# Kernel tuning notes

Hardware: AMD Instinct MI355X
Metric: run time of the kernel (lower is better)

Reference implementation:

```python
import jax, jax.numpy as jnp
import numpy as np

N = 100000          # nodes
E = 1600000         # edges per adjacency (avg degree 16)
DIMS = [256, 128, 64]
ALPHA = 0.8
WD = 1e-4


def setup_inputs() -> dict:
    key = jax.random.key(0)
    ks = jax.random.split(key, 11)
    X = jax.random.normal(ks[0], (N, DIMS[0]), jnp.float32)
    rows = jax.random.randint(ks[1], (E,), 0, N, jnp.int32)
    cols = jax.random.randint(ks[2], (E,), 0, N, jnp.int32)
    prune_rows = jax.random.randint(ks[3], (E,), 0, N, jnp.int32)
    prune_cols = jax.random.randint(ks[4], (E,), 0, N, jnp.int32)
    # learned params (torch.randn init, scaled 0.1 for fp32 numeric headroom)
    W0 = jax.random.normal(ks[5], (DIMS[0], DIMS[1]), jnp.float32) * 0.1
    W1 = jax.random.normal(ks[6], (DIMS[1], DIMS[2]), jnp.float32) * 0.1
    v00 = jax.random.normal(ks[7], (DIMS[1], 1), jnp.float32) * 0.1
    v01 = jax.random.normal(ks[8], (DIMS[1], 1), jnp.float32) * 0.1
    pv00 = jax.random.normal(ks[9], (DIMS[1], 1), jnp.float32) * 0.1
    pv01 = jax.random.normal(ks[10], (DIMS[1], 1), jnp.float32) * 0.1
    return {"X": X, "W0": W0, "W1": W1, "v00": v00, "v01": v01,
            "pv00": pv00, "pv01": pv01, "rows": rows, "cols": cols,
            "prune_rows": prune_rows, "prune_cols": prune_cols}


def _edge_softmax(rows, logits, n):
    # row-wise softmax over sparse edge logits
    m = jax.ops.segment_max(logits, rows, num_segments=n)
    e = jnp.exp(logits - m[rows])
    s = jax.ops.segment_sum(e, rows, num_segments=n)
    return e / s[rows]


def _attention(rows, cols, H, va, vb, n):
    # logit_e = (H @ va)[src_e] + (H @ vb)[dst_e]  (binary adjacency values)
    f1 = (H @ va)[:, 0]
    f2 = (H @ vb)[:, 0]
    return _edge_softmax(rows, f1[rows] + f2[cols], n)


def _spmm(rows, cols, vals, H, n):
    # out[i] = sum_{e: rows[e]==i} vals[e] * H[cols[e]]
    return jax.ops.segment_sum(vals[:, None] * H[cols], rows, num_segments=n)


def reference(X, W0, W1, v00, v01, pv00, pv01, rows, cols, prune_rows, prune_cols):
    n = X.shape[0]
    # ---- encoder ----
    H1 = X @ W0                                   # layer 0 projection
    c = _attention(rows, cols, H1, v00, v01, n)   # C[0]
    pc = _attention(prune_rows, prune_cols, H1, pv00, pv01, n)  # prune_C[0]
    H1a = (1.0 - ALPHA) * _spmm(rows, cols, c, H1, n) \
        + ALPHA * _spmm(prune_rows, prune_cols, pc, H1, n)
    H1a = jax.nn.elu(H1a)                         # nonlinear, layer 0 != last
    H_enc = H1a @ W1                              # layer 1 == last: no attention
    # ---- decoder ----
    D = H_enc @ W1.T                              # layer 1
    D = (1.0 - ALPHA) * _spmm(rows, cols, c, D, n) \
        + ALPHA * _spmm(prune_rows, prune_cols, pc, D, n)
    D = jax.nn.elu(D)                             # nonlinear, layer 1 != 0
    X_ = D @ W0.T                                 # layer 0: plain matmul
    # ---- loss ----
    loss = jnp.sqrt(jnp.sum((X - X_) ** 2)) \
         + WD * (jnp.sum(W0 ** 2) + jnp.sum(W1 ** 2))
    return (loss, H_enc, X_)
```

## Files before the change

### kernel.cpp

```cpp
#include <hip/hip_runtime.h>
#include <math.h>

#define N_NODES 100000
#define N_EDGES 1600000
#define TOT (2 * N_NODES)
#define SCAN_NB 256
#define SCAN_CH 4
#define RPB 25000

static inline int cdiv(long a, long b) { return (int)((a + b - 1) / b); }

typedef unsigned int uint;
typedef unsigned short ushort;
typedef __attribute__((ext_vector_type(8))) short short8v;
typedef __attribute__((ext_vector_type(4))) float f32x4;

__device__ inline float bf2f(uint u) { return __uint_as_float(u << 16); }
__device__ inline ushort f2bf(float f) {
    uint u = __float_as_uint(f);
    uint r = ((u >> 16) & 1u) + 0x7fffu;
    return (ushort)((u + r) >> 16);
}

template <int K, int M, bool AF32, int OUT, bool ELU, bool LOSS>
__global__ __launch_bounds__(256) void gemm_mfma(const void* __restrict__ Av,
                                                 const ushort* __restrict__ Bcm,
                                                 void* __restrict__ Cv,
                                                 void* __restrict__ Cv2,
                                                 const float* __restrict__ Xref,
                                                 float* __restrict__ partial,
                                                 int nrows) {
    constexpr int BM = 128;
    constexpr int KP = K + 8;
    constexpr int NCT = M / 16;
    __shared__ ushort Blds[M * KP];
    __shared__ ushort Alds[BM * 32];
    const int w = threadIdx.x >> 6;
    const int l = threadIdx.x & 63;
    const int rowg = l & 15;
    const int kg = l >> 4;
    const int rbase = blockIdx.x * BM;
    {
        const uint4* src = reinterpret_cast<const uint4*>(Bcm);
        uint4* dst = reinterpret_cast<uint4*>(Blds);
        const int total = M * KP / 8;
        for (int i = threadIdx.x; i < total; i += 256) dst[i] = src[i];
    }
    f32x4 acc[2][NCT] = {};
    for (int k0 = 0; k0 < K; k0 += 32) {
        __syncthreads();
        int r = threadIdx.x >> 1;
        int kk = (threadIdx.x & 1) * 16;
        int rg = min(rbase + r, nrows - 1);
        if (AF32) {
            const float* A = (const float*)Av;
            const float4* src = reinterpret_cast<const float4*>(A + (size_t)rg * K + k0 + kk);
            ushort* dst = &Alds[r * 32 + kk];
#pragma unroll
            for (int q = 0; q < 4; ++q) {
                float4 v = src[q];
                dst[4 * q + 0] = f2bf(v.x); dst[4 * q + 1] = f2bf(v.y);
                dst[4 * q + 2] = f2bf(v.z); dst[4 * q + 3] = f2bf(v.w);
            }
        } else {
            const ushort* A = (const ushort*)Av;
            const uint4* src = reinterpret_cast<const uint4*>(A + (size_t)rg * K + k0 + kk);
            uint4* dst = reinterpret_cast<uint4*>(&Alds[r * 32 + kk]);
            dst[0] = src[0];
            dst[1] = src[1];
        }
        __syncthreads();
#pragma unroll
        for (int rt = 0; rt < 2; ++rt) {
            short8v af = *reinterpret_cast<const short8v*>(
                &Alds[(w * 32 + rt * 16 + rowg) * 32 + kg * 8]);
#pragma unroll
            for (int ct = 0; ct < NCT; ++ct) {
                short8v bf = *reinterpret_cast<const short8v*>(
                    &Blds[(ct * 16 + rowg) * KP + k0 + kg * 8]);
                acc[rt][ct] = __builtin_amdgcn_mfma_f32_16x16x32_bf16(
                    af, bf, acc[rt][ct], 0, 0, 0);
            }
        }
    }
    float lsum = 0.f;
#pragma unroll
    for (int rt = 0; rt < 2; ++rt) {
#pragma unroll
        for (int q = 0; q < 4; ++q) {
            int r = rbase + w * 32 + rt * 16 + kg * 4 + q;
            if (r >= nrows) continue;
#pragma unroll
            for (int ct = 0; ct < NCT; ++ct) {
                float o = acc[rt][ct][q];
                if (ELU) o = o > 0.f ? o : expm1f(o);
                int col = ct * 16 + rowg;
                if (OUT == 0 || OUT == 3) ((float*)Cv)[(size_t)r * M + col] = o;
                if (OUT == 2) ((ushort*)Cv)[(size_t)r * M + col] = f2bf(o);
                if (OUT == 3) ((ushort*)Cv2)[(size_t)r * M + col] = f2bf(o);
                if (LOSS) {
                    float d = o - Xref[(size_t)r * 256 + col];
                    lsum += d * d;
                }
            }
        }
    }
    if (LOSS) {
        __shared__ float smRed[4];
#pragma unroll
        for (int off = 32; off > 0; off >>= 1) lsum += __shfl_down(lsum, off);
        __syncthreads();
        if (l == 0) smRed[w] = lsum;
        __syncthreads();
        if (threadIdx.x == 0)
            partial[blockIdx.x] = smRed[0] + smRed[1] + smRed[2] + smRed[3];
    }
}

__global__ __launch_bounds__(256) void prepB1_kernel(const float* __restrict__ W0,
                                                     ushort* __restrict__ B) {
    int i = blockIdx.x * 256 + threadIdx.x;
    if (i >= 256 * 128) return;
    int k = i / 128, m = i - k * 128;
    B[m * 264 + k] = f2bf(W0[i]);
}
__global__ __launch_bounds__(256) void prepB5_kernel(const float* __restrict__ W1,
                                                     ushort* __restrict__ B) {
    int i = blockIdx.x * 256 + threadIdx.x;
    if (i >= 128 * 64) return;
    int k = i / 64, m = i - k * 64;
    B[m * 136 + k] = f2bf(W1[i]);
}
__global__ __launch_bounds__(256) void prepB7_kernel(const float* __restrict__ W1,
                                                     ushort* __restrict__ B) {
    int i = blockIdx.x * 256 + threadIdx.x;
    if (i >= 128 * 64) return;
    int m = i / 64, k = i - m * 64;
    B[m * 72 + k] = f2bf(W1[i]);
}
__global__ __launch_bounds__(256) void prepB8_kernel(const float* __restrict__ W0,
                                                     ushort* __restrict__ B) {
    int i = blockIdx.x * 256 + threadIdx.x;
    if (i >= 256 * 128) return;
    int m = i / 128, k = i - m * 128;
    B[m * 136 + k] = f2bf(W0[i]);
}

__global__ __launch_bounds__(256) void attn_f4_kernel(const ushort* __restrict__ Hb,
                                                      const float* __restrict__ va,
                                                      const float* __restrict__ vb,
                                                      const float* __restrict__ pva,
                                                      const float* __restrict__ pvb,
                                                      float* __restrict__ f1,
                                                      float* __restrict__ f2,
                                                      float* __restrict__ pf1,
                                                      float* __restrict__ pf2) {
    int wid = (blockIdx.x * 256 + threadIdx.x) >> 6;
    int lane = threadIdx.x & 63;
    if (wid >= N_NODES) return;
    uint hv = reinterpret_cast<const uint*>(Hb + (size_t)wid * 128)[lane];
    float x0 = bf2f(hv & 0xffffu);
    float x1 = bf2f(hv >> 16);
    int k = 2 * lane;
    float a = x0 * va[k] + x1 * va[k + 1];
    float b = x0 * vb[k] + x1 * vb[k + 1];
    float pa = x0 * pva[k] + x1 * pva[k + 1];
    float pb = x0 * pvb[k] + x1 * pvb[k + 1];
#pragma unroll
    for (int off = 32; off > 0; off >>= 1) {
        a += __shfl_down(a, off);
        b += __shfl_down(b, off);
        pa += __shfl_down(pa, off);
        pb += __shfl_down(pb, off);
    }
    if (lane == 0) { f1[wid] = a; f2[wid] = b; pf1[wid] = pa; pf2[wid] = pb; }
}

__global__ __launch_bounds__(256) void hist2_kernel(const int* __restrict__ rows,
                                                    const int* __restrict__ prows,
                                                    int* __restrict__ deg) {
    int e = blockIdx.x * 256 + threadIdx.x;
    if (e >= 2 * N_EDGES) return;
    int b = e < N_EDGES ? rows[e] * 2 : prows[e - N_EDGES] * 2 + 1;
    atomicAdd(&deg[b], 1);
}

__device__ inline int pad8(int d) { return (d + 7) & ~7; }

__global__ __launch_bounds__(256) void scan1_kernel(const int* __restrict__ deg,
                                                    int* __restrict__ bsum) {
    __shared__ int sm[256];
    int base = (blockIdx.x * 256 + threadIdx.x) * SCAN_CH;
    int s = 0;
#pragma unroll
    for (int i = 0; i < SCAN_CH; ++i) {
        int idx = base + i;
        if (idx < TOT) s += pad8(deg[idx]);
    }
    sm[threadIdx.x] = s;
    __syncthreads();
    for (int off = 128; off > 0; off >>= 1) {
        if (threadIdx.x < off) sm[threadIdx.x] += sm[threadIdx.x + off];
        __syncthreads();
    }
    if (threadIdx.x == 0) bsum[blockIdx.x] = sm[0];
}

__global__ void scan2_kernel(int* __restrict__ bsum) {
    if (threadIdx.x != 0) return;
    int run = 0;
    for (int i = 0; i < SCAN_NB; ++i) {
        int t = bsum[i];
        bsum[i] = run;
        run += t;
    }
}

__global__ __launch_bounds__(256) void scan3_kernel(const int* __restrict__ deg,
                                                    const int* __restrict__ bsum,
                                                    int* __restrict__ rp) {
    __shared__ int sm[256];
    int base = (blockIdx.x * 256 + threadIdx.x) * SCAN_CH;
    int s = 0;
#pragma unroll
    for (int i = 0; i < SCAN_CH; ++i) {
        int idx = base + i;
        if (idx < TOT) s += pad8(deg[idx]);
    }
    sm[threadIdx.x] = s;
    __syncthreads();
    if (threadIdx.x == 0) {
        int run = bsum[blockIdx.x];
        for (int t = 0; t < 256; ++t) { int tmp = sm[t]; sm[t] = run; run += tmp; }
    }
    __syncthreads();
    int off = sm[threadIdx.x];
#pragma unroll
    for (int i = 0; i < SCAN_CH; ++i) {
        int idx = base + i;
        if (idx < TOT) { rp[idx] = off; off += pad8(deg[idx]); }
        else if (idx == TOT) rp[idx] = off;
    }
}

__global__ __launch_bounds__(256) void scatter_bucket_kernel(const int* __restrict__ rlist,
                                                             const int* __restrict__ clist,
                                                             int adj, int lo, int hi,
                                                             const int* __restrict__ rp,
                                                             int* __restrict__ cur,
                                                             int* __restrict__ ccol) {
    int e = blockIdx.x * 256 + threadIdx.x;
    if (e >= N_EDGES) return;
    int r0 = rlist[e];
    if (r0 < lo || r0 >= hi) return;
    int b = r0 * 2 + adj;
    int pos = rp[b] + atomicAdd(&cur[b], 1);
    ccol[pos] = clist[e];
}

__global__ __launch_bounds__(256) void edgeval_kernel(const int* __restrict__ rp,
                                                      const int* __restrict__ deg,
                                                      const int* __restrict__ ccol,
                                                      const float* __restrict__ f1,
                                                      const float* __restrict__ f2,
                                                      const float* __restrict__ pf1,
                                                      const float* __restrict__ pf2,
                                                      int2* __restrict__ eg) {
    int b = blockIdx.x * 16 + (threadIdx.x >> 4);
    int sl = threadIdx.x & 15;
    int adj = b & 1, r = b >> 1;
    float f1r = adj ? pf1[r] : f1[r];
    const float* f2t = adj ? pf2 : f2;
    float scale = adj ? 0.8f : 0.2f;
    int j0 = rp[b];
    int realend = j0 + deg[b];
    int pend = rp[b + 1];
    float s = 0.f;
    for (int j = j0 + sl; j < realend; j += 16)
        s += __expf(f1r + f2t[ccol[j]]);
#pragma unroll
    for (int off = 8; off > 0; off >>= 1) s += __shfl_xor(s, off);
    float inv = s > 0.f ? scale / s : 0.f;
    for (int j = j0 + sl; j < pend; j += 16) {
        if (j < realend) {
            int c = ccol[j];
            float wv = __expf(f1r + f2t[c]) * inv;
            eg[j] = make_int2(c, __float_as_int(wv));
        } else {
            eg[j] = make_int2(0, 0);
        }
    }
}

#define SPU 8
__global__ __launch_bounds__(256) void spmm_fused_kernel(const int* __restrict__ rp,
                                                         const int2* __restrict__ eg,
                                                         const ushort* __restrict__ Hb,
                                                         float* __restrict__ out) {
    int r = blockIdx.x * 4 + (threadIdx.x >> 6);
    int lane = threadIdx.x & 63;
    const uint* Hu = reinterpret_cast<const uint*>(Hb);
    float a0 = 0.f, a1 = 0.f;
    int j = rp[2 * r], E = rp[2 * r + 2];
    if (j < E) {
        int2 d[SPU]; uint h[SPU];
#pragma unroll
        for (int u = 0; u < SPU; ++u) d[u] = eg[j + u];
#pragma unroll
        for (int u = 0; u < SPU; ++u) h[u] = Hu[(uint)d[u].x * 64u + lane];
        j += SPU;
        for (; j < E; j += SPU) {
            int2 dn[SPU]; uint hn[SPU];
#pragma unroll
            for (int u = 0; u < SPU; ++u) dn[u] = eg[j + u];
#pragma unroll
            for (int u = 0; u < SPU; ++u) hn[u] = Hu[(uint)dn[u].x * 64u + lane];
#pragma unroll
            for (int u = 0; u < SPU; ++u) {
                float v = __int_as_float(d[u].y);
                a0 += v * bf2f(h[u] & 0xffffu);
                a1 += v * bf2f(h[u] >> 16);
            }
#pragma unroll
            for (int u = 0; u < SPU; ++u) { d[u] = dn[u]; h[u] = hn[u]; }
        }
#pragma unroll
        for (int u = 0; u < SPU; ++u) {
            float v = __int_as_float(d[u].y);
            a0 += v * bf2f(h[u] & 0xffffu);
            a1 += v * bf2f(h[u] >> 16);
        }
    }
    float o0 = a0 > 0.f ? a0 : expm1f(a0);
    float o1 = a1 > 0.f ? a1 : expm1f(a1);
    *reinterpret_cast<float2*>(out + (size_t)r * 128 + 2 * lane) = make_float2(o0, o1);
}

__global__ __launch_bounds__(256) void spmm64_fused_kernel(const int* __restrict__ rp,
                                                           const int2* __restrict__ eg,
                                                           const ushort* __restrict__ Hb,
                                                           float* __restrict__ S) {
    int r = blockIdx.x * 4 + (threadIdx.x >> 6);
    int lane = threadIdx.x & 63;
    float a = 0.f;
    int j = rp[2 * r], E = rp[2 * r + 2];
    if (j < E) {
        int2 d[SPU]; ushort h[SPU];
#pragma unroll
        for (int u = 0; u < SPU; ++u) d[u] = eg[j + u];
#pragma unroll
        for (int u = 0; u < SPU; ++u) h[u] = Hb[(uint)d[u].x * 64u + lane];
        j += SPU;
        for (; j < E; j += SPU) {
            int2 dn[SPU]; ushort hn[SPU];
#pragma unroll
            for (int u = 0; u < SPU; ++u) dn[u] = eg[j + u];
#pragma unroll
            for (int u = 0; u < SPU; ++u) hn[u] = Hb[(uint)dn[u].x * 64u + lane];
#pragma unroll
            for (int u = 0; u < SPU; ++u)
                a += __int_as_float(d[u].y) * bf2f((uint)h[u]);
#pragma unroll
            for (int u = 0; u < SPU; ++u) { d[u] = dn[u]; h[u] = hn[u]; }
        }
#pragma unroll
        for (int u = 0; u < SPU; ++u)
            a += __int_as_float(d[u].y) * bf2f((uint)h[u]);
    }
    S[(size_t)r * 64 + lane] = a;
}

__global__ __launch_bounds__(256) void sq_reduce_kernel(const float* __restrict__ a,
                                                        float* __restrict__ acc, int n) {
    __shared__ float sm[4];
    float s = 0.f;
    for (int i = blockIdx.x * 256 + threadIdx.x; i < n; i += gridDim.x * 256) {
        float d = a[i];
        s += d * d;
    }
#pragma unroll
    for (int off = 32; off > 0; off >>= 1) s += __shfl_down(s, off);
    int lane = threadIdx.x & 63, w = threadIdx.x >> 6;
    if (lane == 0) sm[w] = s;
    __syncthreads();
    if (threadIdx.x == 0) atomicAdd(acc, sm[0] + sm[1] + sm[2] + sm[3]);
}

__global__ __launch_bounds__(256) void partial_reduce_kernel(const float* __restrict__ p,
                                                             int n, float* __restrict__ acc) {
    __shared__ float sm[4];
    float s = 0.f;
    for (int i = threadIdx.x; i < n; i += 256) s += p[i];
#pragma unroll
    for (int off = 32; off > 0; off >>= 1) s += __shfl_down(s, off);
    int lane = threadIdx.x & 63, w = threadIdx.x >> 6;
    if (lane == 0) sm[w] = s;
    __syncthreads();
    if (threadIdx.x == 0) atomicAdd(acc, sm[0] + sm[1] + sm[2] + sm[3]);
}

__global__ void finalize_kernel(const float* __restrict__ acc, float* __restrict__ out) {
    out[0] = sqrtf(acc[0]) + 1e-4f * (acc[1] + acc[2]);
}

extern "C" void kernel_launch(void* const* d_in, const int* in_sizes, int n_in,
                              void* d_out, int out_size, void* d_ws, size_t ws_size,
                              hipStream_t stream) {
    const float* X    = (const float*)d_in[0];
    const float* W0   = (const float*)d_in[1];
    const float* W1   = (const float*)d_in[2];
    const float* v00  = (const float*)d_in[3];
    const float* v01  = (const float*)d_in[4];
    const float* pv00 = (const float*)d_in[5];
    const float* pv01 = (const float*)d_in[6];
    const int* rows   = (const int*)d_in[7];
    const int* cols   = (const int*)d_in[8];
    const int* prows  = (const int*)d_in[9];
    const int* pcols  = (const int*)d_in[10];

    float* out  = (float*)d_out;
    float* Henc = out + 1;
    float* Xrec = out + 1 + (size_t)N_NODES * 64;

    ushort* bufAh  = (ushort*)(out + 6400004);
    float*  S      = out + 6400004;
    int*    ccol   = (int*)(out + 12800004);
    int2*   eg     = (int2*)(out + 17600004);
    ushort* HencB  = (ushort*)(out + 27200004);
    int*    deg    = (int*)(out + 28800004);
    int*    cur    = deg + TOT;

    float* ws   = (float*)d_ws;
    float* bufB = ws;
    ushort* bufBh = (ushort*)bufB;
    float* f1   = bufB + (size_t)N_NODES * 128;
    float* f2   = f1 + N_NODES;
    float* pf1  = f2 + N_NODES;
    float* pf2  = pf1 + N_NODES;
    float* acc  = pf2 + N_NODES;
    ushort* B1cm = (ushort*)(acc + 4);
    ushort* B5cm = B1cm + 128 * 264;
    ushort* B7cm = B5cm + 64 * 136;
    ushort* B8cm = B7cm + 128 * 72;
    int*   rp   = (int*)(B8cm + 256 * 136);
    int*   bsum = rp + TOT + 1;
    float* partial = (float*)(bsum + SCAN_NB);

    const int n = N_NODES;
    const int EG = cdiv(N_EDGES, 256);
    const int EG2 = cdiv(2 * (long)N_EDGES, 256);

    prepB1_kernel<<<cdiv(256 * 128, 256), 256, 0, stream>>>(W0, B1cm);
    prepB5_kernel<<<cdiv(128 * 64, 256), 256, 0, stream>>>(W1, B5cm);
    prepB7_kernel<<<cdiv(128 * 64, 256), 256, 0, stream>>>(W1, B7cm);
    prepB8_kernel<<<cdiv(256 * 128, 256), 256, 0, stream>>>(W0, B8cm);

    gemm_mfma<256, 128, true, 2, false, false><<<cdiv(n, 128), 256, 0, stream>>>(
        X, B1cm, bufAh, nullptr, nullptr, nullptr, n);

    hipMemsetAsync(deg, 0, 2 * (size_t)TOT * sizeof(int), stream);
    hipMemsetAsync(acc, 0, 4 * sizeof(float), stream);

    attn_f4_kernel<<<cdiv(n, 4), 256, 0, stream>>>(bufAh, v00, v01, pv00, pv01,
                                                   f1, f2, pf1, pf2);

    hist2_kernel<<<EG2, 256, 0, stream>>>(rows, prows, deg);
    scan1_kernel<<<SCAN_NB, 256, 0, stream>>>(deg, bsum);
    scan2_kernel<<<1, 64, 0, stream>>>(bsum);
    scan3_kernel<<<SCAN_NB, 256, 0, stream>>>(deg, bsum, rp);
    for (int p = 0; p < 4; ++p)
        scatter_bucket_kernel<<<EG, 256, 0, stream>>>(rows, cols, 0,
                                                      p * RPB, (p + 1) * RPB,
                                                      rp, cur, ccol);
    for (int p = 0; p < 4; ++p)
        scatter_bucket_kernel<<<EG, 256, 0, stream>>>(prows, pcols, 1,
                                                      p * RPB, (p + 1) * RPB,
                                                      rp, cur, ccol);
    edgeval_kernel<<<cdiv(TOT, 16), 256, 0, stream>>>(rp, deg, ccol,
                                                      f1, f2, pf1, pf2, eg);

    spmm_fused_kernel<<<n / 4, 256, 0, stream>>>(rp, eg, bufAh, bufB);

    gemm_mfma<128, 64, true, 3, false, false><<<cdiv(n, 128), 256, 0, stream>>>(
        bufB, B5cm, Henc, HencB, nullptr, nullptr, n);

    spmm64_fused_kernel<<<n / 4, 256, 0, stream>>>(rp, eg, HencB, S);

    gemm_mfma<64, 128, true, 2, true, false><<<cdiv(n, 128), 256, 0, stream>>>(
        S, B7cm, bufBh, nullptr, nullptr, nullptr, n);

    gemm_mfma<128, 256, false, 0, false, true><<<cdiv(n, 128), 256, 0, stream>>>(
        bufBh, B8cm, Xrec, nullptr, X, partial, n);

    partial_reduce_kernel<<<1, 256, 0, stream>>>(partial, cdiv(n, 128), acc + 0);
    sq_reduce_kernel<<<16, 256, 0, stream>>>(W0, acc + 1, 256 * 128);
    sq_reduce_kernel<<<4, 256, 0, stream>>>(W1, acc + 2, 128 * 64);
    finalize_kernel<<<1, 1, 0, stream>>>(acc, out);
}
```

Before: 799.7 us.

## Fuse edge-value computation into scatter and defer softmax normalization to SpMM

Removes the separate edgeval pass. The scatter kernel now computes exp(f1+f2) per edge, writes (col, value) pairs into the CSR buffer, and atomically accumulates per-row sums. Both SpMM kernels then apply the 0.2/0.8-scaled reciprocal of the row sum, picking between the two adjacencies per 8-edge chunk. The four weight-prep kernels are merged into one launch, and the W1 square-sum now shares an accumulator with W0. In exchange it adds float atomics per edge, a memset over the edge buffer to zero the padding, and a dead self-copy line left in the prep kernel.

```diff
diff --git a/kernel.cpp b/kernel.cpp
--- a/kernel.cpp
+++ b/kernel.cpp
@@ -7,6 +7,7 @@
 #define SCAN_NB 256
 #define SCAN_CH 4
 #define RPB 25000
+#define EG_CAP 4800000
 
 static inline int cdiv(long a, long b) { return (int)((a + b - 1) / b); }
 
@@ -117,33 +118,35 @@
     }
 }
 
-__global__ __launch_bounds__(256) void prepB1_kernel(const float* __restrict__ W0,
-                                                     ushort* __restrict__ B) {
+__global__ __launch_bounds__(256) void prep_all_kernel(const float* __restrict__ W0,
+                                                       const float* __restrict__ W1,
+                                                       ushort* __restrict__ B1,
+                                                       ushort* __restrict__ B5,
+                                                       ushort* __restrict__ B7,
+                                                       ushort* __restrict__ B8) {
     int i = blockIdx.x * 256 + threadIdx.x;
-    if (i >= 256 * 128) return;
-    int k = i / 128, m = i - k * 128;
-    B[m * 264 + k] = f2bf(W0[i]);
-}
-__global__ __launch_bounds__(256) void prepB5_kernel(const float* __restrict__ W1,
-                                                     ushort* __restrict__ B) {
-    int i = blockIdx.x * 256 + threadIdx.x;
-    if (i >= 128 * 64) return;
-    int k = i / 64, m = i - k * 64;
-    B[m * 136 + k] = f2bf(W1[i]);
-}
-__global__ __launch_bounds__(256) void prepB7_kernel(const float* __restrict__ W1,
-                                                     ushort* __restrict__ B) {
-    int i = blockIdx.x * 256 + threadIdx.x;
-    if (i >= 128 * 64) return;
-    int m = i / 64, k = i - m * 64;
-    B[m * 72 + k] = f2bf(W1[i]);
-}
-__global__ __launch_bounds__(256) void prepB8_kernel(const float* __restrict__ W0,
-                                                     ushort* __restrict__ B) {
-    int i = blockIdx.x * 256 + threadIdx.x;
-    if (i >= 256 * 128) return;
-    int m = i / 128, k = i - m * 128;
-    B[m * 136 + k] = f2bf(W0[i]);
+    if (i < 32768) {
+        int k = i / 128, m = i - k * 128;
+        B1[m * 264 + k] = f2bf(W0[i]);
+        int m8 = k, k8 = m;
+        B8[i % 1 * 0 + 0] = B8[0];
+    }
+    if (i < 32768) {
+        int k = i / 128, m = i - k * 128;
+        B1[m * 264 + k] = f2bf(W0[i]);
+    } else if (i < 65536) {
+        int j = i - 32768;
+        int m = j / 128, k = j - m * 128;
+        B8[m * 136 + k] = f2bf(W0[j]);
+    } else if (i < 73728) {
+        int j = i - 65536;
+        int k = j / 64, m = j - k * 64;
+        B5[m * 136 + k] = f2bf(W1[j]);
+    } else if (i < 81920) {
+        int j = i - 73728;
+        int m = j / 64, k = j - m * 64;
+        B7[m * 72 + k] = f2bf(W1[j]);
+    }
 }
 
 __global__ __launch_bounds__(256) void attn_f4_kernel(const ushort* __restrict__ Hb,
@@ -243,90 +246,69 @@
     }
 }
 
-__global__ __launch_bounds__(256) void scatter_bucket_kernel(const int* __restrict__ rlist,
-                                                             const int* __restrict__ clist,
-                                                             int adj, int lo, int hi,
-                                                             const int* __restrict__ rp,
-                                                             int* __restrict__ cur,
-                                                             int* __restrict__ ccol) {
+__global__ __launch_bounds__(256) void scatter_fused_kernel(const int* __restrict__ rlist,
+                                                            const int* __restrict__ clist,
+                                                            int adj, int lo, int hi,
+                                                            const float* __restrict__ f1t,
+                                                            const float* __restrict__ f2t,
+                                                            const int* __restrict__ rp,
+                                                            int* __restrict__ cur,
+                                                            int2* __restrict__ eg,
+                                                            float* __restrict__ sums) {
     int e = blockIdx.x * 256 + threadIdx.x;
     if (e >= N_EDGES) return;
     int r0 = rlist[e];
     if (r0 < lo || r0 >= hi) return;
+    int c = clist[e];
+    float v = __expf(f1t[r0] + f2t[c]);
     int b = r0 * 2 + adj;
     int pos = rp[b] + atomicAdd(&cur[b], 1);
-    ccol[pos] = clist[e];
-}
-
-__global__ __launch_bounds__(256) void edgeval_kernel(const int* __restrict__ rp,
-                                                      const int* __restrict__ deg,
-                                                      const int* __restrict__ ccol,
-                                                      const float* __restrict__ f1,
-                                                      const float* __restrict__ f2,
-                                                      const float* __restrict__ pf1,
-                                                      const float* __restrict__ pf2,
-                                                      int2* __restrict__ eg) {
-    int b = blockIdx.x * 16 + (threadIdx.x >> 4);
-    int sl = threadIdx.x & 15;
-    int adj = b & 1, r = b >> 1;
-    float f1r = adj ? pf1[r] : f1[r];
-    const float* f2t = adj ? pf2 : f2;
-    float scale = adj ? 0.8f : 0.2f;
-    int j0 = rp[b];
-    int realend = j0 + deg[b];
-    int pend = rp[b + 1];
-    float s = 0.f;
-    for (int j = j0 + sl; j < realend; j += 16)
-        s += __expf(f1r + f2t[ccol[j]]);
-#pragma unroll
-    for (int off = 8; off > 0; off >>= 1) s += __shfl_xor(s, off);
-    float inv = s > 0.f ? scale / s : 0.f;
-    for (int j = j0 + sl; j < pend; j += 16) {
-        if (j < realend) {
-            int c = ccol[j];
-            float wv = __expf(f1r + f2t[c]) * inv;
-            eg[j] = make_int2(c, __float_as_int(wv));
-        } else {
-            eg[j] = make_int2(0, 0);
-        }
-    }
+    eg[pos] = make_int2(c, __float_as_int(v));
+    atomicAdd(&sums[b], v);
 }
 
 #define SPU 8
 __global__ __launch_bounds__(256) void spmm_fused_kernel(const int* __restrict__ rp,
                                                          const int2* __restrict__ eg,
+                                                         const float* __restrict__ sums,
                                                          const ushort* __restrict__ Hb,
                                                          float* __restrict__ out) {
     int r = blockIdx.x * 4 + (threadIdx.x >> 6);
     int lane = threadIdx.x & 63;
     const uint* Hu = reinterpret_cast<const uint*>(Hb);
     float a0 = 0.f, a1 = 0.f;
-    int j = rp[2 * r], E = rp[2 * r + 2];
-    if (j < E) {
+    int j0 = rp[2 * r], mid = rp[2 * r + 1], E = rp[2 * r + 2];
+    float s0 = sums[2 * r], s1 = sums[2 * r + 1];
+    float inv0 = s0 > 0.f ? 0.2f / s0 : 0.f;
+    float inv1 = s1 > 0.f ? 0.8f / s1 : 0.f;
+    if (j0 < E) {
         int2 d[SPU]; uint h[SPU];
 #pragma unroll
-        for (int u = 0; u < SPU; ++u) d[u] = eg[j + u];
+        for (int u = 0; u < SPU; ++u) d[u] = eg[j0 + u];
 #pragma unroll
         for (int u = 0; u < SPU; ++u) h[u] = Hu[(uint)d[u].x * 64u + lane];
-        j += SPU;
-        for (; j < E; j += SPU) {
+        int jc = j0;
+        for (int j = j0 + SPU; j < E; j += SPU) {
             int2 dn[SPU]; uint hn[SPU];
 #pragma unroll
             for (int u = 0; u < SPU; ++u) dn[u] = eg[j + u];
 #pragma unroll
             for (int u = 0; u < SPU; ++u) hn[u] = Hu[(uint)dn[u].x * 64u + lane];
+            float winv = jc < mid ? inv0 : inv1;
 #pragma unroll
             for (int u = 0; u < SPU; ++u) {
-                float v = __int_as_float(d[u].y);
+                float v = __int_as_float(d[u].y) * winv;
                 a0 += v * bf2f(h[u] & 0xffffu);
                 a1 += v * bf2f(h[u] >> 16);
             }
 #pragma unroll
             for (int u = 0; u < SPU; ++u) { d[u] = dn[u]; h[u] = hn[u]; }
-        }
+            jc = j;
+        }
+        float winv = jc < mid ? inv0 : inv1;
 #pragma unroll
         for (int u = 0; u < SPU; ++u) {
-            float v = __int_as_float(d[u].y);
+            float v = __int_as_float(d[u].y) * winv;
             a0 += v * bf2f(h[u] & 0xffffu);
             a1 += v * bf2f(h[u] >> 16);
         }
@@ -338,34 +320,41 @@
 
 __global__ __launch_bounds__(256) void spmm64_fused_kernel(const int* __restrict__ rp,
                                                            const int2* __restrict__ eg,
+                                                           const float* __restrict__ sums,
                                                            const ushort* __restrict__ Hb,
                                                            float* __restrict__ S) {
     int r = blockIdx.x * 4 + (threadIdx.x >> 6);
     int lane = threadIdx.x & 63;
     float a = 0.f;
-    int j = rp[2 * r], E = rp[2 * r + 2];
-    if (j < E) {
+    int j0 = rp[2 * r], mid = rp[2 * r + 1], E = rp[2 * r + 2];
+    float s0 = sums[2 * r], s1 = sums[2 * r + 1];
+    float inv0 = s0 > 0.f ? 0.2f / s0 : 0.f;
+    float inv1 = s1 > 0.f ? 0.8f / s1 : 0.f;
+    if (j0 < E) {
         int2 d[SPU]; ushort h[SPU];
 #pragma unroll
-        for (int u = 0; u < SPU; ++u) d[u] = eg[j + u];
+        for (int u = 0; u < SPU; ++u) d[u] = eg[j0 + u];
 #pragma unroll
         for (int u = 0; u < SPU; ++u) h[u] = Hb[(uint)d[u].x * 64u + lane];
-        j += SPU;
-        for (; j < E; j += SPU) {
+        int jc = j0;
+        for (int j = j0 + SPU; j < E; j += SPU) {
             int2 dn[SPU]; ushort hn[SPU];
 #pragma unroll
             for (int u = 0; u < SPU; ++u) dn[u] = eg[j + u];
 #pragma unroll
             for (int u = 0; u < SPU; ++u) hn[u] = Hb[(uint)dn[u].x * 64u + lane];
+            float winv = jc < mid ? inv0 : inv1;
 #pragma unroll
             for (int u = 0; u < SPU; ++u)
-                a += __int_as_float(d[u].y) * bf2f((uint)h[u]);
+                a += __int_as_float(d[u].y) * winv * bf2f((uint)h[u]);
 #pragma unroll
             for (int u = 0; u < SPU; ++u) { d[u] = dn[u]; h[u] = hn[u]; }
-        }
+            jc = j;
+        }
+        float winv = jc < mid ? inv0 : inv1;
 #pragma unroll
         for (int u = 0; u < SPU; ++u)
-            a += __int_as_float(d[u].y) * bf2f((uint)h[u]);
+            a += __int_as_float(d[u].y) * winv * bf2f((uint)h[u]);
     }
     S[(size_t)r * 64 + lane] = a;
 }
@@ -400,7 +389,7 @@
 }
 
 __global__ void finalize_kernel(const float* __restrict__ acc, float* __restrict__ out) {
-    out[0] = sqrtf(acc[0]) + 1e-4f * (acc[1] + acc[2]);
+    out[0] = sqrtf(acc[0]) + 1e-4f * acc[1];
 }
 
 extern "C" void kernel_launch(void* const* d_in, const int* in_sizes, int n_in,
@@ -424,11 +413,11 @@
 
     ushort* bufAh  = (ushort*)(out + 6400004);
     float*  S      = out + 6400004;
-    int*    ccol   = (int*)(out + 12800004);
-    int2*   eg     = (int2*)(out + 17600004);
-    ushort* HencB  = (ushort*)(out + 27200004);
-    int*    deg    = (int*)(out + 28800004);
+    int2*   eg     = (int2*)(out + 12800004);
+    ushort* HencB  = (ushort*)(out + 22400004);
+    int*    deg    = (int*)(out + 25600004);
     int*    cur    = deg + TOT;
+    float*  sums   = (float*)(cur + TOT);
 
     float* ws   = (float*)d_ws;
     float* bufB = ws;
@@ -450,16 +439,14 @@
     const int EG = cdiv(N_EDGES, 256);
     const int EG2 = cdiv(2 * (long)N_EDGES, 256);
 
-    prepB1_kernel<<<cdiv(256 * 128, 256), 256, 0, stream>>>(W0, B1cm);
-    prepB5_kernel<<<cdiv(128 * 64, 256), 256, 0, stream>>>(W1, B5cm);
-    prepB7_kernel<<<cdiv(128 * 64, 256), 256, 0, stream>>>(W1, B7cm);
-    prepB8_kernel<<<cdiv(256 * 128, 256), 256, 0, stream>>>(W0, B8cm);
+    prep_all_kernel<<<cdiv(81920, 256), 256, 0, stream>>>(W0, W1, B1cm, B5cm, B7cm, B8cm);
 
     gemm_mfma<256, 128, true, 2, false, false><<<cdiv(n, 128), 256, 0, stream>>>(
         X, B1cm, bufAh, nullptr, nullptr, nullptr, n);
 
-    hipMemsetAsync(deg, 0, 2 * (size_t)TOT * sizeof(int), stream);
+    hipMemsetAsync(deg, 0, 3 * (size_t)TOT * sizeof(int), stream);
     hipMemsetAsync(acc, 0, 4 * sizeof(float), stream);
+    hipMemsetAsync(eg, 0, (size_t)EG_CAP * sizeof(int2), stream);
 
     attn_f4_kernel<<<cdiv(n, 4), 256, 0, stream>>>(bufAh, v00, v01, pv00, pv01,
                                                    f1, f2, pf1, pf2);
@@ -469,22 +456,20 @@
     scan2_kernel<<<1, 64, 0, stream>>>(bsum);
     scan3_kernel<<<SCAN_NB, 256, 0, stream>>>(deg, bsum, rp);
     for (int p = 0; p < 4; ++p)
-        scatter_bucket_kernel<<<EG, 256, 0, stream>>>(rows, cols, 0,
-                                                      p * RPB, (p + 1) * RPB,
-                                                      rp, cur, ccol);
+        scatter_fused_kernel<<<EG, 256, 0, stream>>>(rows, cols, 0,
+                                                     p * RPB, (p + 1) * RPB,
+                                                     f1, f2, rp, cur, eg, sums);
     for (int p = 0; p < 4; ++p)
-        scatter_bucket_kernel<<<EG, 256, 0, stream>>>(prows, pcols, 1,
-                                                      p * RPB, (p + 1) * RPB,
-                                                      rp, cur, ccol);
-    edgeval_kernel<<<cdiv(TOT, 16), 256, 0, stream>>>(rp, deg, ccol,
-                                                      f1, f2, pf1, pf2, eg);
-
-    spmm_fused_kernel<<<n / 4, 256, 0, stream>>>(rp, eg, bufAh, bufB);
+        scatter_fused_kernel<<<EG, 256, 0, stream>>>(prows, pcols, 1,
+                                                     p * RPB, (p + 1) * RPB,
+                                                     pf1, pf2, rp, cur, eg, sums);
+
+    spmm_fused_kernel<<<n / 4, 256, 0, stream>>>(rp, eg, sums, bufAh, bufB);
 
     gemm_mfma<128, 64, true, 3, false, false><<<cdiv(n, 128), 256, 0, stream>>>(
         bufB, B5cm, Henc, HencB, nullptr, nullptr, n);
 
-    spmm64_fused_kernel<<<n / 4, 256, 0, stream>>>(rp, eg, HencB, S);
+    spmm64_fused_kernel<<<n / 4, 256, 0, stream>>>(rp, eg, sums, HencB, S);
 
     gemm_mfma<64, 128, true, 2, true, false><<<cdiv(n, 128), 256, 0, stream>>>(
         S, B7cm, bufBh, nullptr, nullptr, nullptr, n);
@@ -494,6 +479,6 @@
 
     partial_reduce_kernel<<<1, 256, 0, stream>>>(partial, cdiv(n, 128), acc + 0);
     sq_reduce_kernel<<<16, 256, 0, stream>>>(W0, acc + 1, 256 * 128);
-    sq_reduce_kernel<<<4, 256, 0, stream>>>(W1, acc + 2, 128 * 64);
+    sq_reduce_kernel<<<4, 256, 0, stream>>>(W1, acc + 1, 128 * 64);
     finalize_kernel<<<1, 1, 0, stream>>>(acc, out);
 }
```

After: 936.2 us. +17.1%, slower.
